# Kernel optimization log

Measured on AMD Instinct MI355X. Metric: run time of the kernel, lower is better.

The kernel has to match this reference:

```python
import jax, jax.numpy as jnp
import numpy as np

B, S, D, H = 2, 2048, 1024, 16
DK = D // H

def setup_inputs() -> dict:
    key = jax.random.key(0)
    ks = jax.random.split(key, 11)
    s = 1.0 / np.sqrt(D)
    return {
        "q": jax.random.normal(ks[0], (B, S, D), jnp.float32),
        "k": jax.random.normal(ks[1], (B, S, D), jnp.float32),
        "v": jax.random.normal(ks[2], (B, S, D), jnp.float32),
        "Wq": jax.random.normal(ks[3], (D, D), jnp.float32) * s,
        "bq": jax.random.normal(ks[4], (D,), jnp.float32) * s,
        "Wk": jax.random.normal(ks[5], (D, D), jnp.float32) * s,
        "bk": jax.random.normal(ks[6], (D,), jnp.float32) * s,
        "Wv": jax.random.normal(ks[7], (D, D), jnp.float32) * s,
        "bv": jax.random.normal(ks[8], (D,), jnp.float32) * s,
        "Wo": jax.random.normal(ks[9], (D, D), jnp.float32) * s,
        "bo": jax.random.normal(ks[10], (D,), jnp.float32) * s,
    }

def reference(q, k, v, Wq, bq, Wk, bk, Wv, bv, Wo, bo):
    # Linear projections, then split into heads: [B,S,D] -> [B,H,S,DK]
    def heads(x, W, b):
        y = x @ W.T + b
        return y.reshape(B, S, H, DK).transpose(0, 2, 1, 3)
    qh = heads(q, Wq, bq)
    kh = heads(k, Wk, bk)
    vh = heads(v, Wv, bv)
    scores = jnp.einsum('bhsd,bhtd->bhst', qh, kh) / jnp.sqrt(jnp.float32(DK))
    attn = jax.nn.softmax(scores, axis=-1)
    out = jnp.einsum('bhst,bhtd->bhsd', attn, vh)  # [B,H,S,DK]
    out = out.transpose(0, 2, 1, 3).reshape(B, S, D)
    return out @ Wo.T + bo
```

## Files before the change

### kernel.cpp

```cpp
#include <hip/hip_runtime.h>
#include <stdint.h>

#define B_  2
#define S_  2048
#define D_  1024
#define H_  16
#define DK_ 64

typedef unsigned short u16;
typedef __attribute__((ext_vector_type(8))) __bf16 bf16x8;
typedef __attribute__((ext_vector_type(4))) float f32x4;
typedef __attribute__((ext_vector_type(4))) short short4v;
typedef __attribute__((ext_vector_type(8))) short short8v;

static __device__ __forceinline__ u16 f2bf(float f) {
    union { float f; uint32_t u; } v; v.f = f;
    return (u16)((v.u + 0x7fffu + ((v.u >> 16) & 1u)) >> 16);
}
static __device__ __forceinline__ uint32_t pk2bf(float x, float y) {
    return (uint32_t)f2bf(x) | ((uint32_t)f2bf(y) << 16);
}
static __device__ __forceinline__ uint32_t cvtpk_bf16(float lo, float hi) {
    uint32_t r; asm("v_cvt_pk_bf16_f32 %0, %1, %2" : "=v"(r) : "v"(lo), "v"(hi));
    return r;
}
static __device__ __forceinline__ float exp2f_fast(float x) {
    float r; asm("v_exp_f32 %0, %1" : "=v"(r) : "v"(x)); return r;
}

#define GLOAD16(gp, lp) \
    __builtin_amdgcn_global_load_lds((const __attribute__((address_space(1))) void*)(gp), \
                                     (__attribute__((address_space(3))) void*)(lp), 16, 0, 0)

static __device__ __forceinline__ int swz(int lin) { return lin ^ ((lin >> 3) & 7); }

static __device__ __forceinline__ int xcd_swz(int bid, int cpx) {
    return (bid & 7) * cpx + (bid >> 3);
}

__global__ __launch_bounds__(256) void cast_all_kernel(
        const float* __restrict__ q, const float* __restrict__ k, const float* __restrict__ v,
        const float* __restrict__ Wq, const float* __restrict__ Wk,
        const float* __restrict__ Wv, const float* __restrict__ Wo,
        u16* __restrict__ qb, u16* __restrict__ kb, u16* __restrict__ vb,
        u16* __restrict__ Wqb, u16* __restrict__ Wkb, u16* __restrict__ Wvb,
        u16* __restrict__ Wob) {
    int blk = blockIdx.x;
    const float* src; u16* dst; int off;
    if (blk < 2048)      { src = q;  dst = qb;  off = blk; }
    else if (blk < 4096) { src = k;  dst = kb;  off = blk - 2048; }
    else if (blk < 6144) { src = v;  dst = vb;  off = blk - 4096; }
    else if (blk < 6656) { src = Wq; dst = Wqb; off = blk - 6144; }
    else if (blk < 7168) { src = Wk; dst = Wkb; off = blk - 6656; }
    else if (blk < 7680) { src = Wv; dst = Wvb; off = blk - 7168; }
    else                 { src = Wo; dst = Wob; off = blk - 7680; }
    int i = (off * 256 + threadIdx.x) * 8;
    float4 a = *(const float4*)(src + i);
    float4 b = *(const float4*)(src + i + 4);
    uint4 r;
    r.x = pk2bf(a.x, a.y); r.y = pk2bf(a.z, a.w);
    r.z = pk2bf(b.x, b.y); r.w = pk2bf(b.z, b.w);
    *(uint4*)(void*)(dst + i) = r;
}

__device__ __forceinline__ void gemm128_compute(
        const u16* __restrict__ X, const u16* __restrict__ W,
        int m0, int n0, u16* lds, f32x4 acc[4][4]) {
    const int tid = threadIdx.x, lane = tid & 63, w = tid >> 6;
    const int wm = w >> 1, wn = w & 1;
    u16* As = lds;
    u16* Bs = lds + 8192;

    auto stage = [&](int bi, int kt) {
#pragma unroll
        for (int r = 0; r < 2; ++r) {
            int s = tid + (r << 8);
            int lin = s ^ ((s >> 3) & 7);
            int row = lin >> 2, ch = lin & 3;
            GLOAD16(X + (size_t)(m0 + row) * 1024 + (kt << 5) + (ch << 3),
                    (char*)(As + bi * 4096) + ((r << 8) + (w << 6)) * 16);
            GLOAD16(W + (size_t)(n0 + row) * 1024 + (kt << 5) + (ch << 3),
                    (char*)(Bs + bi * 4096) + ((r << 8) + (w << 6)) * 16);
        }
    };

    stage(0, 0);
    asm volatile("s_waitcnt vmcnt(0)" ::: "memory");
    __syncthreads();
#pragma unroll 1
    for (int kt = 0; kt < 32; ++kt) {
        const int cur = kt & 1;
        if (kt < 31) stage(cur ^ 1, kt + 1);
        const char* Ab = (const char*)(As + cur * 4096);
        const char* Bb = (const char*)(Bs + cur * 4096);
        bf16x8 a[4], b[4];
#pragma unroll
        for (int f = 0; f < 4; ++f) {
            int rowa = wm * 64 + f * 16 + (lane & 15);
            a[f] = *(const bf16x8*)(Ab + swz(rowa * 4 + (lane >> 4)) * 16);
            int rowb = wn * 64 + f * 16 + (lane & 15);
            b[f] = *(const bf16x8*)(Bb + swz(rowb * 4 + (lane >> 4)) * 16);
        }
#pragma unroll
        for (int fm = 0; fm < 4; ++fm)
#pragma unroll
            for (int fn = 0; fn < 4; ++fn)
                acc[fm][fn] = __builtin_amdgcn_mfma_f32_16x16x32_bf16(
                    a[fm], b[fn], acc[fm][fn], 0, 0, 0);
        __syncthreads();
    }
}

__device__ __forceinline__ void stage_half(const u16* __restrict__ src,
        int R0, int kt, u16* dst, int tid) {
#pragma unroll
    for (int r = 0; r < 2; ++r) {
        int s = tid + (r << 9);
        int lin = s ^ ((s >> 3) & 7);
        int row = lin >> 3, ch = lin & 7;
        GLOAD16(src + (size_t)(R0 + row) * 1024 + (kt << 6) + (ch << 3),
                (char*)dst + ((r << 9) + ((tid >> 6) << 6)) * 16);
    }
}

#define VM4  asm volatile("s_waitcnt vmcnt(4)" ::: "memory")
#define VM0  asm volatile("s_waitcnt vmcnt(0)" ::: "memory")

#define PHASE(QQ, MP, LOADB, STAGE_STMT, VM_STMT)                                \
    {                                                                            \
        bf16x8 afr[2][2];                                                        \
        if (LOADB) {                                                             \
            _Pragma("unroll") for (int fn = 0; fn < 4; ++fn)                     \
            _Pragma("unroll") for (int ks = 0; ks < 2; ++ks) {                   \
                int lin = (brow0 + fn * 16 + (lane & 15)) * 8 + ks * 4 + (lane >> 4); \
                bfr[fn][ks] = *(const bf16x8*)(Bhb[QQ] + swz(lin) * 16);         \
            }                                                                    \
        }                                                                        \
        _Pragma("unroll") for (int fo = 0; fo < 2; ++fo)                         \
        _Pragma("unroll") for (int ks = 0; ks < 2; ++ks) {                       \
            int lin = ((MP) * 32 + fo * 16 + (lane & 15)) * 8 + ks * 4 + (lane >> 4); \
            afr[fo][ks] = *(const bf16x8*)(Ahb[QQ] + swz(lin) * 16);             \
        }                                                                        \
        STAGE_STMT;                                                              \
        VM_STMT;                                                                 \
        __builtin_amdgcn_s_barrier();                                            \
        __builtin_amdgcn_sched_barrier(0);                                       \
        __builtin_amdgcn_s_setprio(1);                                           \
        _Pragma("unroll") for (int fo = 0; fo < 2; ++fo)                         \
        _Pragma("unroll") for (int ks = 0; ks < 2; ++ks)                         \
        _Pragma("unroll") for (int fn = 0; fn < 4; ++fn)                         \
            acc[(MP) * 2 + fo][fn] = __builtin_amdgcn_mfma_f32_16x16x32_bf16(    \
                afr[fo][ks], bfr[fn][ks], acc[(MP) * 2 + fo][fn], 0, 0, 0);      \
        __builtin_amdgcn_s_setprio(0);                                           \
        __builtin_amdgcn_s_barrier();                                            \
        __builtin_amdgcn_sched_barrier(0);                                       \
    }

__global__ __launch_bounds__(512, 2) void qkv256_kernel(
        const u16* __restrict__ qX, const u16* __restrict__ kX, const u16* __restrict__ vX,
        const u16* __restrict__ Wq, const u16* __restrict__ Wk, const u16* __restrict__ Wv,
        const float* __restrict__ bq, const float* __restrict__ bk, const float* __restrict__ bv,
        u16* __restrict__ qo, u16* __restrict__ ko, u16* __restrict__ vt) {
    __shared__ __align__(16) u16 lds[65536];
    const int tid = threadIdx.x, lane = tid & 63, w = tid >> 6;
    const int wm = w >> 2, wn = w & 3;
    const int lg = xcd_swz(blockIdx.x, 24);
    const int which = lg >> 6;
    const int rem = lg & 63;
    const int n0 = (rem >> 4) << 8;
    const int m0 = (rem & 15) << 8;
    const u16* X = which == 0 ? qX : (which == 1 ? kX : vX);
    const u16* W = which == 0 ? Wq : (which == 1 ? Wk : Wv);
    const float* bias = which == 0 ? bq : (which == 1 ? bk : bv);

    u16* Abase = lds;
    u16* Bbase = lds + 32768;

    stage_half(X, m0,        0, Abase + 0,             tid);
    stage_half(X, m0 + 128,  0, Abase + 8192,          tid);
    stage_half(W, n0,        0, Bbase + 0,             tid);
    stage_half(W, n0 + 128,  0, Bbase + 8192,          tid);
    stage_half(W, n0,        1, Bbase + 16384,         tid);
    stage_half(W, n0 + 128,  1, Bbase + 16384 + 8192,  tid);
    VM4;
    __builtin_amdgcn_s_barrier();
    __builtin_amdgcn_sched_barrier(0);

    f32x4 acc[8][4] = {};
    bf16x8 bfr[4][2];
    const char* Ahb[2] = { (const char*)(Abase + wm * 8192),
                           (const char*)(Abase + 16384 + wm * 8192) };
    const char* Bhb[2] = { (const char*)(Bbase + (wn >> 1) * 8192),
                           (const char*)(Bbase + 16384 + (wn >> 1) * 8192) };
    const int brow0 = (wn & 1) * 64;

#pragma unroll 1
    for (int i = 0; i < 8; ++i) {
        const int t0 = 2 * i, t1 = 2 * i + 1;
        const bool nl = (i < 7);
        PHASE(0, 0, true,  stage_half(X, m0,       t1,     Abase + 16384,        tid), (void)0);
        PHASE(0, 1, false, stage_half(X, m0 + 128, t1,     Abase + 16384 + 8192, tid), (void)0);
        PHASE(0, 2, false, if (nl) stage_half(W, n0,       t0 + 2, Bbase + 0,    tid), (void)0);
        PHASE(0, 3, false, if (nl) stage_half(W, n0 + 128, t0 + 2, Bbase + 8192, tid),
              if (nl) { VM4; } else { VM0; });
        PHASE(1, 0, true,  if (nl) stage_half(X, m0,       t0 + 2, Abase + 0,    tid), (void)0);
        PHASE(1, 1, false, if (nl) stage_half(X, m0 + 128, t0 + 2, Abase + 8192, tid), (void)0);
        PHASE(1, 2, false, if (nl) stage_half(W, n0,       t1 + 2, Bbase + 16384, tid), (void)0);
        PHASE(1, 3, false, if (nl) stage_half(W, n0 + 128, t1 + 2, Bbase + 16384 + 8192, tid),
              if (nl) { VM4; });
    }

    if (which < 2) {
        u16* out = which == 0 ? qo : ko;
        const float scale = which == 0 ? 0.1803368801111883f : 1.0f;
#pragma unroll
        for (int fn = 0; fn < 4; ++fn) {
            int n = n0 + wn * 64 + fn * 16 + (lane & 15);
            float bb = bias[n];
            int h = n >> 6, dk = n & 63;
#pragma unroll
            for (int fm = 0; fm < 8; ++fm)
#pragma unroll
                for (int j = 0; j < 4; ++j) {
                    int m = m0 + wm * 128 + fm * 16 + (lane >> 4) * 4 + j;
                    int b = m >> 11, s = m & 2047;
                    out[((size_t)(b * H_ + h) * S_ + s) * DK_ + dk] =
                        f2bf((acc[fm][fn][j] + bb) * scale);
                }
        }
    } else {
        __syncthreads();
        u16* wl = lds + w * 8192;
#pragma unroll
        for (int fn = 0; fn < 4; ++fn) {
            int dk = fn * 16 + (lane & 15);
            float bb = bias[n0 + wn * 64 + dk];
            int xr = (dk & 7) << 3;
#pragma unroll
            for (int fm = 0; fm < 8; ++fm) {
                int sl = fm * 16 + (lane >> 4) * 4;
                short4v p;
#pragma unroll
                for (int j = 0; j < 4; ++j) p[j] = (short)f2bf(acc[fm][fn][j] + bb);
                *(short4v*)(void*)&wl[dk * 128 + (sl ^ xr)] = p;
            }
        }
        int mrow = m0 + wm * 128;
        int b = mrow >> 11, sbase = mrow & 2047;
        int h = (n0 >> 6) + wn;
        u16* dst = vt + ((size_t)(b * H_ + h) * DK_) * S_ + sbase;
#pragma unroll
        for (int oc = 0; oc < 8; ++oc)
#pragma unroll
            for (int ic = 0; ic < 2; ++ic) {
                int dk = oc * 8 + (lane >> 3);
                int sc = ic * 8 + (lane & 7);
                short8v vv = *(const short8v*)(const void*)
                    &wl[dk * 128 + ((sc * 8) ^ ((dk & 7) << 3))];
                *(short8v*)(void*)(dst + (size_t)dk * S_ + sc * 8) = vv;
            }
    }
}

__global__ __launch_bounds__(256) void oproj_kernel(
        const u16* __restrict__ X, const u16* __restrict__ W,
        const float* __restrict__ bias, float* __restrict__ out) {
    __shared__ __align__(16) u16 lds[16384];
    const int bid = xcd_swz(blockIdx.x, 32);
    const int m0 = (bid >> 3) << 7;
    const int n0 = (bid & 7) << 7;
    f32x4 acc[4][4] = {};
    gemm128_compute(X, W, m0, n0, lds, acc);

    const int lane = threadIdx.x & 63, w = threadIdx.x >> 6;
    const int wm = w >> 1, wn = w & 1;
#pragma unroll
    for (int fn = 0; fn < 4; ++fn) {
        int n = n0 + wn * 64 + fn * 16 + (lane & 15);
        float bb = bias[n];
#pragma unroll
        for (int fm = 0; fm < 4; ++fm)
#pragma unroll
            for (int j = 0; j < 4; ++j) {
                int m = m0 + wm * 64 + fm * 16 + (lane >> 4) * 4 + j;
                out[(size_t)m * 1024 + n] = acc[fm][fn][j] + bb;
            }
    }
}

__global__ __launch_bounds__(256) void attn_kernel(
        const u16* __restrict__ qh, const u16* __restrict__ kh,
        const u16* __restrict__ Vt, u16* __restrict__ ao) {
    __shared__ __align__(16) u16 Qs[8192];
    __shared__ __align__(16) u16 Ks[2][4096];
    __shared__ __align__(16) u16 Vs[2][4096];
    __shared__ __align__(16) u16 Ps[8192];

    const int tid = threadIdx.x, lane = tid & 63, w = tid >> 6;
    const int lg = xcd_swz(blockIdx.x, 64);
    const int bh = lg >> 4, qt = lg & 15;
    const u16* qg = qh + ((size_t)bh * S_ + qt * 128) * DK_;
    const u16* kg = kh + (size_t)bh * S_ * DK_;
    const u16* vg = Vt + (size_t)bh * DK_ * S_;

    auto stageKV = [&](int bi, int kt) {
#pragma unroll
        for (int r = 0; r < 2; ++r) {
            int s = tid + (r << 8);
            int lin = s ^ ((s >> 3) & 7);
            int row = lin >> 3, ch = lin & 7;
            GLOAD16(kg + (size_t)(kt * 64 + row) * 64 + (ch << 3),
                    (char*)(&Ks[bi][0]) + ((r << 8) + (w << 6)) * 16);
            GLOAD16(vg + (size_t)row * S_ + kt * 64 + (ch << 3),
                    (char*)(&Vs[bi][0]) + ((r << 8) + (w << 6)) * 16);
        }
    };

#pragma unroll
    for (int r = 0; r < 4; ++r) {
        int s = tid + (r << 8);
        int lin = s ^ ((s >> 3) & 7);
        int row = lin >> 3, ch = lin & 7;
        GLOAD16(qg + row * 64 + (ch << 3), (char*)Qs + ((r << 8) + (w << 6)) * 16);
    }
    stageKV(0, 0);
    asm volatile("s_waitcnt vmcnt(0)" ::: "memory");
    __syncthreads();

    bf16x8 qf[2][2];
#pragma unroll
    for (int fn = 0; fn < 2; ++fn)
#pragma unroll
        for (int ks = 0; ks < 2; ++ks) {
            int row = w * 32 + fn * 16 + (lane & 15);
            qf[fn][ks] = *(const bf16x8*)((const char*)Qs +
                          swz(row * 8 + ks * 4 + (lane >> 4)) * 16);
        }

    union { short8v s; bf16x8 b; } onesu;
#pragma unroll
    for (int i = 0; i < 8; ++i) onesu.s[i] = 0x3F80;
    const bf16x8 onesf = onesu.b;

    f32x4 acc[2][4] = {};
    f32x4 accl[2] = {};
    u16* Pw = Ps + w * 2048;

#pragma unroll 1
    for (int kt = 0; kt < 32; ++kt) {
        const int cur = kt & 1;
        if (kt < 31) stageKV(cur ^ 1, kt + 1);
        const char* Kb = (const char*)&Ks[cur][0];
        const char* Vb = (const char*)&Vs[cur][0];

        f32x4 st[4][2] = {};
#pragma unroll
        for (int ks = 0; ks < 2; ++ks) {
            bf16x8 kf[4];
#pragma unroll
            for (int fm = 0; fm < 4; ++fm) {
                int row = fm * 16 + (lane & 15);
                kf[fm] = *(const bf16x8*)(Kb + swz(row * 8 + ks * 4 + (lane >> 4)) * 16);
            }
            __builtin_amdgcn_s_setprio(1);
#pragma unroll
            for (int fm = 0; fm < 4; ++fm)
#pragma unroll
                for (int fn = 0; fn < 2; ++fn)
                    st[fm][fn] = __builtin_amdgcn_mfma_f32_16x16x32_bf16(
                        kf[fm], qf[fn][ks], st[fm][fn], 0, 0, 0);
            __builtin_amdgcn_s_setprio(0);
        }

#pragma unroll
        for (int fm = 0; fm < 4; ++fm)
#pragma unroll
            for (int fn = 0; fn < 2; ++fn) {
                float e0 = exp2f_fast(st[fm][fn][0]);
                float e1 = exp2f_fast(st[fm][fn][1]);
                float e2 = exp2f_fast(st[fm][fn][2]);
                float e3 = exp2f_fast(st[fm][fn][3]);
                uint2 pk; pk.x = cvtpk_bf16(e0, e1); pk.y = cvtpk_bf16(e2, e3);
                int qrow = fn * 16 + (lane & 15);
                int g = lane >> 4;
                int slot = qrow * 8 + fm * 2 + (g >> 1);
                int ph = slot ^ (qrow & 7);
                *(uint2*)((char*)Pw + ph * 16 + (g & 1) * 8) = pk;
            }

#pragma unroll
        for (int ks2 = 0; ks2 < 2; ++ks2) {
            bf16x8 pa[2], vb2[4];
#pragma unroll
            for (int fm2 = 0; fm2 < 2; ++fm2) {
                int row = fm2 * 16 + (lane & 15);
                pa[fm2] = *(const bf16x8*)((const char*)Pw +
                            swz(row * 8 + ks2 * 4 + (lane >> 4)) * 16);
            }
#pragma unroll
            for (int fn2 = 0; fn2 < 4; ++fn2) {
                int row = fn2 * 16 + (lane & 15);
                vb2[fn2] = *(const bf16x8*)(Vb + swz(row * 8 + ks2 * 4 + (lane >> 4)) * 16);
            }
            __builtin_amdgcn_s_setprio(1);
#pragma unroll
            for (int fm2 = 0; fm2 < 2; ++fm2) {
#pragma unroll
                for (int fn2 = 0; fn2 < 4; ++fn2)
                    acc[fm2][fn2] = __builtin_amdgcn_mfma_f32_16x16x32_bf16(
                        pa[fm2], vb2[fn2], acc[fm2][fn2], 0, 0, 0);
                accl[fm2] = __builtin_amdgcn_mfma_f32_16x16x32_bf16(
                    pa[fm2], onesf, accl[fm2], 0, 0, 0);
            }
            __builtin_amdgcn_s_setprio(0);
        }
        __syncthreads();
    }

    const int b = bh >> 4, h = bh & 15;
#pragma unroll
    for (int fm2 = 0; fm2 < 2; ++fm2) {
        float inv[4];
#pragma unroll
        for (int j = 0; j < 4; ++j)
            inv[j] = 1.0f / accl[fm2][j];
#pragma unroll
        for (int fn2 = 0; fn2 < 4; ++fn2)
#pragma unroll
            for (int j = 0; j < 4; ++j) {
                int srow = qt * 128 + w * 32 + fm2 * 16 + (lane >> 4) * 4 + j;
                int col = h * 64 + fn2 * 16 + (lane & 15);
                ao[((size_t)b * S_ + srow) * D_ + col] = f2bf(acc[fm2][fn2][j] * inv[j]);
            }
    }
}

extern "C" void kernel_launch(void* const* d_in, const int* in_sizes, int n_in,
                              void* d_out, int out_size, void* d_ws, size_t ws_size,
                              hipStream_t stream) {
    const float* q  = (const float*)d_in[0];
    const float* k  = (const float*)d_in[1];
    const float* v  = (const float*)d_in[2];
    const float* Wq = (const float*)d_in[3];
    const float* bq = (const float*)d_in[4];
    const float* Wk = (const float*)d_in[5];
    const float* bk = (const float*)d_in[6];
    const float* Wv = (const float*)d_in[7];
    const float* bv = (const float*)d_in[8];
    const float* Wo = (const float*)d_in[9];
    const float* bo = (const float*)d_in[10];

    char* ws = (char*)d_ws;
    u16* qb  = (u16*)(ws);
    u16* kb  = (u16*)(ws + (8u  << 20));
    u16* vb  = (u16*)(ws + (16u << 20));
    u16* Wqb = (u16*)(ws + (24u << 20));
    u16* Wkb = (u16*)(ws + (26u << 20));
    u16* Wvb = (u16*)(ws + (28u << 20));
    u16* Wob = (u16*)(ws + (30u << 20));
    u16* qhb = (u16*)(ws + (32u << 20));
    u16* khb = (u16*)(ws + (40u << 20));
    u16* Vtb = (u16*)(ws + (48u << 20));
    u16* aob = kb;

    cast_all_kernel<<<8192, 256, 0, stream>>>(q, k, v, Wq, Wk, Wv, Wo,
                                              qb, kb, vb, Wqb, Wkb, Wvb, Wob);

    qkv256_kernel<<<192, 512, 0, stream>>>(
        qb, kb, vb, Wqb, Wkb, Wvb, bq, bk, bv, qhb, khb, Vtb);

    attn_kernel<<<512, 256, 0, stream>>>(qhb, khb, Vtb, aob);

    oproj_kernel<<<256, 256, 0, stream>>>(aob, Wob, bo, (float*)d_out);
}
```

Baseline: 120.1 us.

## Switch attention to 32x32 MFMA and keep P in registers via permlane swap

Rewrites the attention inner loop to use 32x32x16 bf16 MFMA tiles instead of 16x16x32. The exponentiated scores are repacked into the A-operand layout in registers with v_permlane32_swap, so the per-wave P buffer in shared memory and its LDS round trip are removed. Launch bounds now request two blocks per SM. The risk is register pressure from the 16-wide accumulators and correctness of the lane permutation and output row mapping.

New measurement: 117.1 us. 1.03x faster.

```diff
diff --git a/kernel.cpp b/kernel.cpp
--- a/kernel.cpp
+++ b/kernel.cpp
@@ -10,6 +10,7 @@
 typedef unsigned short u16;
 typedef __attribute__((ext_vector_type(8))) __bf16 bf16x8;
 typedef __attribute__((ext_vector_type(4))) float f32x4;
+typedef __attribute__((ext_vector_type(16))) float f32x16;
 typedef __attribute__((ext_vector_type(4))) short short4v;
 typedef __attribute__((ext_vector_type(8))) short short8v;
 
@@ -288,15 +289,15 @@
     }
 }
 
-__global__ __launch_bounds__(256) void attn_kernel(
+__global__ __launch_bounds__(256, 2) void attn_kernel(
         const u16* __restrict__ qh, const u16* __restrict__ kh,
         const u16* __restrict__ Vt, u16* __restrict__ ao) {
     __shared__ __align__(16) u16 Qs[8192];
     __shared__ __align__(16) u16 Ks[2][4096];
     __shared__ __align__(16) u16 Vs[2][4096];
-    __shared__ __align__(16) u16 Ps[8192];
 
     const int tid = threadIdx.x, lane = tid & 63, w = tid >> 6;
+    const int l31 = lane & 31, hh = lane >> 5;
     const int lg = xcd_swz(blockIdx.x, 64);
     const int bh = lg >> 4, qt = lg & 15;
     const u16* qg = qh + ((size_t)bh * S_ + qt * 128) * DK_;
@@ -327,24 +328,20 @@
     asm volatile("s_waitcnt vmcnt(0)" ::: "memory");
     __syncthreads();
 
-    bf16x8 qf[2][2];
-#pragma unroll
-    for (int fn = 0; fn < 2; ++fn)
-#pragma unroll
-        for (int ks = 0; ks < 2; ++ks) {
-            int row = w * 32 + fn * 16 + (lane & 15);
-            qf[fn][ks] = *(const bf16x8*)((const char*)Qs +
-                          swz(row * 8 + ks * 4 + (lane >> 4)) * 16);
-        }
+    bf16x8 qf[4];
+#pragma unroll
+    for (int c = 0; c < 4; ++c) {
+        int row = w * 32 + l31;
+        qf[c] = *(const bf16x8*)((const char*)Qs + swz(row * 8 + c * 2 + hh) * 16);
+    }
 
     union { short8v s; bf16x8 b; } onesu;
 #pragma unroll
     for (int i = 0; i < 8; ++i) onesu.s[i] = 0x3F80;
     const bf16x8 onesf = onesu.b;
 
-    f32x4 acc[2][4] = {};
-    f32x4 accl[2] = {};
-    u16* Pw = Ps + w * 2048;
+    f32x16 acc[2] = {};
+    f32x16 accl = {};
 
 #pragma unroll 1
     for (int kt = 0; kt < 32; ++kt) {
@@ -353,85 +350,81 @@
         const char* Kb = (const char*)&Ks[cur][0];
         const char* Vb = (const char*)&Vs[cur][0];
 
-        f32x4 st[4][2] = {};
-#pragma unroll
-        for (int ks = 0; ks < 2; ++ks) {
+        f32x16 st[2] = {};
+#pragma unroll
+        for (int kb = 0; kb < 2; ++kb) {
             bf16x8 kf[4];
 #pragma unroll
-            for (int fm = 0; fm < 4; ++fm) {
-                int row = fm * 16 + (lane & 15);
-                kf[fm] = *(const bf16x8*)(Kb + swz(row * 8 + ks * 4 + (lane >> 4)) * 16);
+            for (int c = 0; c < 4; ++c) {
+                int row = kb * 32 + l31;
+                kf[c] = *(const bf16x8*)(Kb + swz(row * 8 + c * 2 + hh) * 16);
             }
             __builtin_amdgcn_s_setprio(1);
 #pragma unroll
-            for (int fm = 0; fm < 4; ++fm)
-#pragma unroll
-                for (int fn = 0; fn < 2; ++fn)
-                    st[fm][fn] = __builtin_amdgcn_mfma_f32_16x16x32_bf16(
-                        kf[fm], qf[fn][ks], st[fm][fn], 0, 0, 0);
+            for (int c = 0; c < 4; ++c)
+                st[kb] = __builtin_amdgcn_mfma_f32_32x32x16_bf16(
+                    kf[c], qf[c], st[kb], 0, 0, 0);
             __builtin_amdgcn_s_setprio(0);
         }
 
-#pragma unroll
-        for (int fm = 0; fm < 4; ++fm)
-#pragma unroll
-            for (int fn = 0; fn < 2; ++fn) {
-                float e0 = exp2f_fast(st[fm][fn][0]);
-                float e1 = exp2f_fast(st[fm][fn][1]);
-                float e2 = exp2f_fast(st[fm][fn][2]);
-                float e3 = exp2f_fast(st[fm][fn][3]);
-                uint2 pk; pk.x = cvtpk_bf16(e0, e1); pk.y = cvtpk_bf16(e2, e3);
-                int qrow = fn * 16 + (lane & 15);
-                int g = lane >> 4;
-                int slot = qrow * 8 + fm * 2 + (g >> 1);
-                int ph = slot ^ (qrow & 7);
-                *(uint2*)((char*)Pw + ph * 16 + (g & 1) * 8) = pk;
-            }
-
-#pragma unroll
-        for (int ks2 = 0; ks2 < 2; ++ks2) {
-            bf16x8 pa[2], vb2[4];
-#pragma unroll
-            for (int fm2 = 0; fm2 < 2; ++fm2) {
-                int row = fm2 * 16 + (lane & 15);
-                pa[fm2] = *(const bf16x8*)((const char*)Pw +
-                            swz(row * 8 + ks2 * 4 + (lane >> 4)) * 16);
-            }
-#pragma unroll
-            for (int fn2 = 0; fn2 < 4; ++fn2) {
-                int row = fn2 * 16 + (lane & 15);
-                vb2[fn2] = *(const bf16x8*)(Vb + swz(row * 8 + ks2 * 4 + (lane >> 4)) * 16);
+        bf16x8 pa[4];
+#pragma unroll
+        for (int c = 0; c < 4; ++c) {
+            const int kb = c >> 1, o = (c & 1) * 8;
+            float e0 = exp2f_fast(st[kb][o + 0]);
+            float e1 = exp2f_fast(st[kb][o + 1]);
+            float e2 = exp2f_fast(st[kb][o + 2]);
+            float e3 = exp2f_fast(st[kb][o + 3]);
+            float e4 = exp2f_fast(st[kb][o + 4]);
+            float e5 = exp2f_fast(st[kb][o + 5]);
+            float e6 = exp2f_fast(st[kb][o + 6]);
+            float e7 = exp2f_fast(st[kb][o + 7]);
+            uint32_t u0 = cvtpk_bf16(e0, e1);
+            uint32_t u1 = cvtpk_bf16(e2, e3);
+            uint32_t u2 = cvtpk_bf16(e4, e5);
+            uint32_t u3 = cvtpk_bf16(e6, e7);
+            asm volatile("v_permlane32_swap_b32 %0, %1" : "+v"(u0), "+v"(u2));
+            asm volatile("v_permlane32_swap_b32 %0, %1" : "+v"(u1), "+v"(u3));
+            union { uint32_t u[4]; bf16x8 v; } pu;
+            pu.u[0] = u0; pu.u[1] = u1; pu.u[2] = u2; pu.u[3] = u3;
+            pa[c] = pu.v;
+        }
+
+        __builtin_amdgcn_s_setprio(1);
+#pragma unroll
+        for (int c = 0; c < 4; ++c)
+            accl = __builtin_amdgcn_mfma_f32_32x32x16_bf16(
+                pa[c], onesf, accl, 0, 0, 0);
+        __builtin_amdgcn_s_setprio(0);
+#pragma unroll
+        for (int nb = 0; nb < 2; ++nb) {
+            bf16x8 vf[4];
+#pragma unroll
+            for (int c = 0; c < 4; ++c) {
+                int row = nb * 32 + l31;
+                vf[c] = *(const bf16x8*)(Vb + swz(row * 8 + c * 2 + hh) * 16);
             }
             __builtin_amdgcn_s_setprio(1);
 #pragma unroll
-            for (int fm2 = 0; fm2 < 2; ++fm2) {
-#pragma unroll
-                for (int fn2 = 0; fn2 < 4; ++fn2)
-                    acc[fm2][fn2] = __builtin_amdgcn_mfma_f32_16x16x32_bf16(
-                        pa[fm2], vb2[fn2], acc[fm2][fn2], 0, 0, 0);
-                accl[fm2] = __builtin_amdgcn_mfma_f32_16x16x32_bf16(
-                    pa[fm2], onesf, accl[fm2], 0, 0, 0);
-            }
+            for (int c = 0; c < 4; ++c)
+                acc[nb] = __builtin_amdgcn_mfma_f32_32x32x16_bf16(
+                    pa[c], vf[c], acc[nb], 0, 0, 0);
             __builtin_amdgcn_s_setprio(0);
         }
         __syncthreads();
     }
 
-    const int b = bh >> 4, h = bh & 15;
-#pragma unroll
-    for (int fm2 = 0; fm2 < 2; ++fm2) {
-        float inv[4];
-#pragma unroll
-        for (int j = 0; j < 4; ++j)
-            inv[j] = 1.0f / accl[fm2][j];
-#pragma unroll
-        for (int fn2 = 0; fn2 < 4; ++fn2)
-#pragma unroll
-            for (int j = 0; j < 4; ++j) {
-                int srow = qt * 128 + w * 32 + fm2 * 16 + (lane >> 4) * 4 + j;
-                int col = h * 64 + fn2 * 16 + (lane & 15);
-                ao[((size_t)b * S_ + srow) * D_ + col] = f2bf(acc[fm2][fn2][j] * inv[j]);
-            }
+    const int bb = bh >> 4, hd = bh & 15;
+#pragma unroll
+    for (int r = 0; r < 16; ++r) {
+        float inv = 1.0f / accl[r];
+        int ql = (r & 3) + 8 * (r >> 2) + 4 * hh;
+        int srow = qt * 128 + w * 32 + ql;
+#pragma unroll
+        for (int nb = 0; nb < 2; ++nb) {
+            int col = hd * 64 + nb * 32 + l31;
+            ao[((size_t)bb * S_ + srow) * D_ + col] = f2bf(acc[nb][r] * inv);
+        }
     }
 }
 
```
